# Kernel tuning notes

Measured on AMD Instinct MI355X. Metric: run time of the kernel, lower is better.

Reference implementation:

```python
import jax, jax.numpy as jnp
import numpy as np

D_MODEL = 1024
D_CODEX = 64
CODEX_SIZE = 8192
BETA = 1.0
EPS_NORM = 1e-12
EPS_LN = 1e-5


def l2norm(x):
    # F.normalize(p=2, dim=-1, eps=1e-12): x / max(||x||, eps)
    n = jnp.sqrt(jnp.sum(x * x, axis=-1, keepdims=True))
    return x / jnp.maximum(n, EPS_NORM)


def setup_inputs() -> dict:
    key = jax.random.key(0)
    ks = jax.random.split(key, 8)
    B, S = 4, 2048
    Z = jax.random.normal(ks[0], (B, S, D_MODEL), dtype=jnp.float32)
    W1 = 0.02 * jax.random.normal(ks[1], (D_MODEL, D_MODEL), dtype=jnp.float32)
    b1 = jnp.zeros((D_MODEL,), dtype=jnp.float32)
    W2 = 0.02 * jax.random.normal(ks[2], (D_MODEL, D_CODEX), dtype=jnp.float32)
    b2 = jnp.zeros((D_CODEX,), dtype=jnp.float32)
    codex = l2norm(jax.random.normal(ks[3], (CODEX_SIZE, D_CODEX), dtype=jnp.float32))
    ln_w = jnp.ones((D_CODEX,), dtype=jnp.float32)
    ln_b = jnp.zeros((D_CODEX,), dtype=jnp.float32)
    Wp = 0.02 * jax.random.normal(ks[4], (D_CODEX, D_MODEL), dtype=jnp.float32)
    bp = jnp.zeros((D_MODEL,), dtype=jnp.float32)
    return {"Z": Z, "W1": W1, "b1": b1, "W2": W2, "b2": b2,
            "codex": codex, "ln_w": ln_w, "ln_b": ln_b, "Wp": Wp, "bp": bp}


def reference(Z, W1, b1, W2, b2, codex, ln_w, ln_b, Wp, bp):
    # pre_proj: Linear -> Tanh -> Linear, then l2-normalize into codex space
    Z_e = jnp.tanh(Z @ W1 + b1) @ W2 + b2            # (B, S, d_codex)
    Z_e = l2norm(Z_e)
    flat = Z_e.reshape(-1, D_CODEX)                  # (N, d_codex)
    # squared-L2 distances: |z|^2 + |c|^2 - 2 z.c
    dists = (jnp.sum(flat * flat, axis=-1, keepdims=True)
             + jnp.sum(codex * codex, axis=-1)[None, :]
             - 2.0 * jnp.einsum('nd,cd->nc', flat, codex))  # (N, K)
    idxs = jnp.argmin(dists, axis=-1).reshape(Z_e.shape[:-1])  # (B, S)
    codex_probs = jax.nn.one_hot(idxs, CODEX_SIZE, dtype=Z_e.dtype)  # (B, S, K)
    Z_q = codex[idxs]                                 # (B, S, d_codex)
    # commitment loss (codex is an EMA buffer, no gradient through it)
    loss = BETA * jnp.mean((jax.lax.stop_gradient(Z_q) - Z_e) ** 2)
    # straight-through estimator
    Z_q = Z_e + jax.lax.stop_gradient(Z_q - Z_e)
    # layernorm over d_codex
    mu = jnp.mean(Z_q, axis=-1, keepdims=True)
    var = jnp.mean((Z_q - mu) ** 2, axis=-1, keepdims=True)
    Z_q = (Z_q - mu) * jax.lax.rsqrt(var + EPS_LN) * ln_w + ln_b
    # post_proj back to d_model
    Z_q = Z_q @ Wp + bp                               # (B, S, d_model)
    return Z_q, loss, codex_probs
```

## Files before the change

kernel.cpp:

```cpp
#include <hip/hip_runtime.h>
#include <math.h>
#include <stdint.h>

#define N_TOK   8192
#define DMODEL  1024
#define DCODEX  64
#define KCODES  8192

__global__ __launch_bounds__(256) void codenorm_kernel(const float* __restrict__ codex,
                                                       float* __restrict__ cn2) {
    int k = blockIdx.x * 256 + threadIdx.x;
    const float4* p = (const float4*)(codex + (size_t)k * DCODEX);
    float s = 0.f;
#pragma unroll
    for (int i = 0; i < 16; ++i) {
        float4 v = p[i];
        s += v.x * v.x + v.y * v.y + v.z * v.z + v.w * v.w;
    }
    cn2[k] = s;
}

__global__ __launch_bounds__(256) void gemm1_tanh_kernel(const float* __restrict__ Z,
                                                         const float* __restrict__ W1,
                                                         const float* __restrict__ b1,
                                                         float* __restrict__ H) {
    __shared__ float As[32][132];
    __shared__ float Bs[32][132];
    const int tid = threadIdx.x;
    const int row0 = blockIdx.x * 128;
    const int col0 = blockIdx.y * 128;
    const int ty = tid >> 4, tx = tid & 15;

    float acc[8][8];
#pragma unroll
    for (int i = 0; i < 8; ++i)
#pragma unroll
        for (int j = 0; j < 8; ++j) acc[i][j] = 0.f;

    for (int k0 = 0; k0 < DMODEL; k0 += 32) {
        __syncthreads();
#pragma unroll
        for (int t = 0; t < 4; ++t) {
            int q = tid + t * 256;
            int r = q >> 3, kc = (q & 7) * 4;
            float4 v = *(const float4*)(Z + (size_t)(row0 + r) * DMODEL + k0 + kc);
            As[kc + 0][r] = v.x; As[kc + 1][r] = v.y;
            As[kc + 2][r] = v.z; As[kc + 3][r] = v.w;
        }
#pragma unroll
        for (int t = 0; t < 4; ++t) {
            int q = tid + t * 256;
            int kk = q >> 5, c4 = (q & 31) * 4;
            *(float4*)&Bs[kk][c4] =
                *(const float4*)(W1 + (size_t)(k0 + kk) * DMODEL + col0 + c4);
        }
        __syncthreads();
#pragma unroll
        for (int k = 0; k < 32; ++k) {
            float a[8], b[8];
            *(float4*)&a[0] = *(const float4*)&As[k][ty * 4];
            *(float4*)&a[4] = *(const float4*)&As[k][64 + ty * 4];
            *(float4*)&b[0] = *(const float4*)&Bs[k][tx * 4];
            *(float4*)&b[4] = *(const float4*)&Bs[k][64 + tx * 4];
#pragma unroll
            for (int i = 0; i < 8; ++i)
#pragma unroll
                for (int j = 0; j < 8; ++j)
                    acc[i][j] = fmaf(a[i], b[j], acc[i][j]);
        }
    }

    float bv[8];
    *(float4*)&bv[0] = *(const float4*)(b1 + col0 + tx * 4);
    *(float4*)&bv[4] = *(const float4*)(b1 + col0 + 64 + tx * 4);
#pragma unroll
    for (int half = 0; half < 2; ++half)
#pragma unroll
        for (int i = 0; i < 4; ++i) {
            int r = row0 + half * 64 + ty * 4 + i;
            float o[8];
#pragma unroll
            for (int j = 0; j < 8; ++j) o[j] = tanhf(acc[half * 4 + i][j] + bv[j]);
            *(float4*)(H + (size_t)r * DMODEL + col0 + tx * 4)      = *(float4*)&o[0];
            *(float4*)(H + (size_t)r * DMODEL + col0 + 64 + tx * 4) = *(float4*)&o[4];
        }
}

__global__ __launch_bounds__(256) void gemm2_norm_kernel(const float* __restrict__ H,
                                                         const float* __restrict__ W2,
                                                         const float* __restrict__ b2,
                                                         float* __restrict__ Ze) {
    __shared__ float As[64][36];
    __shared__ float Bs[64][68];
    const int tid = threadIdx.x;
    const int row0 = blockIdx.x * 32;
    const int ty = tid >> 4, tx = tid & 15;

    float acc[2][4];
#pragma unroll
    for (int i = 0; i < 2; ++i)
#pragma unroll
        for (int j = 0; j < 4; ++j) acc[i][j] = 0.f;

    for (int k0 = 0; k0 < DMODEL; k0 += 64) {
        __syncthreads();
#pragma unroll
        for (int t = 0; t < 2; ++t) {
            int q = tid + t * 256;
            int r = q >> 4, k4 = (q & 15) * 4;
            float4 v = *(const float4*)(H + (size_t)(row0 + r) * DMODEL + k0 + k4);
            As[k4 + 0][r] = v.x; As[k4 + 1][r] = v.y;
            As[k4 + 2][r] = v.z; As[k4 + 3][r] = v.w;
        }
#pragma unroll
        for (int t = 0; t < 4; ++t) {
            int q = tid + t * 256;
            int kk = q >> 4, c4 = (q & 15) * 4;
            *(float4*)&Bs[kk][c4] = *(const float4*)(W2 + (size_t)(k0 + kk) * DCODEX + c4);
        }
        __syncthreads();
#pragma unroll
        for (int k = 0; k < 64; ++k) {
            float2 a = *(const float2*)&As[k][ty * 2];
            float4 b = *(const float4*)&Bs[k][tx * 4];
            float bw[4] = {b.x, b.y, b.z, b.w};
#pragma unroll
            for (int j = 0; j < 4; ++j) {
                acc[0][j] = fmaf(a.x, bw[j], acc[0][j]);
                acc[1][j] = fmaf(a.y, bw[j], acc[1][j]);
            }
        }
    }
    float4 b2v4 = *(const float4*)(b2 + tx * 4);
    float b2v[4] = {b2v4.x, b2v4.y, b2v4.z, b2v4.w};
#pragma unroll
    for (int i = 0; i < 2; ++i) {
        float e[4];
#pragma unroll
        for (int j = 0; j < 4; ++j) e[j] = acc[i][j] + b2v[j];
        float ss = e[0] * e[0] + e[1] * e[1] + e[2] * e[2] + e[3] * e[3];
        ss += __shfl_xor(ss, 8, 64);
        ss += __shfl_xor(ss, 4, 64);
        ss += __shfl_xor(ss, 2, 64);
        ss += __shfl_xor(ss, 1, 64);
        float nrm = fmaxf(sqrtf(ss), 1e-12f);
        float o[4];
#pragma unroll
        for (int j = 0; j < 4; ++j) o[j] = e[j] / nrm;
        *(float4*)(Ze + (size_t)(row0 + ty * 2 + i) * DCODEX + tx * 4) = *(float4*)&o[0];
    }
}

__device__ __forceinline__ unsigned fenc(float f) {
    unsigned u = __float_as_uint(f);
    return (u & 0x80000000u) ? ~u : (u | 0x80000000u);
}

__global__ __launch_bounds__(256) void dist_argmin_kernel(const float* __restrict__ Ze,
                                                          const float* __restrict__ codex,
                                                          const float* __restrict__ cn2,
                                                          unsigned long long* __restrict__ gbest) {
    __shared__ float Zs[64][132];
    __shared__ float Cs[32][132];
    __shared__ unsigned long long red[128];
    const int tid = threadIdx.x;
    const int row0 = blockIdx.x * 128;
    const int strip0 = blockIdx.y * 1024;
    const int ty = tid >> 4, tx = tid & 15;

    if (tid < 128) red[tid] = 0xFFFFFFFFFFFFFFFFull;
#pragma unroll
    for (int t = 0; t < 8; ++t) {
        int q = tid + t * 256;
        int r = q >> 4, d4 = (q & 15) * 4;
        float4 v = *(const float4*)(Ze + (size_t)(row0 + r) * DCODEX + d4);
        Zs[d4 + 0][r] = v.x; Zs[d4 + 1][r] = v.y;
        Zs[d4 + 2][r] = v.z; Zs[d4 + 3][r] = v.w;
    }

    float bv[8];
    int bi[8];
#pragma unroll
    for (int i = 0; i < 8; ++i) { bv[i] = INFINITY; bi[i] = 0; }

    for (int c0 = 0; c0 < 1024; c0 += 128) {
        const int cbase = strip0 + c0;
        float cn[8];
        *(float4*)&cn[0] = *(const float4*)(cn2 + cbase + tx * 4);
        *(float4*)&cn[4] = *(const float4*)(cn2 + cbase + 64 + tx * 4);
        float s[8][8];
#pragma unroll
        for (int i = 0; i < 8; ++i)
#pragma unroll
            for (int j = 0; j < 8; ++j) s[i][j] = 0.f;

        for (int h = 0; h < 2; ++h) {
            __syncthreads();
#pragma unroll
            for (int t = 0; t < 4; ++t) {
                int q = tid + t * 256;
                int c = q >> 3, d4 = (q & 7) * 4;
                float4 v = *(const float4*)(codex + (size_t)(cbase + c) * DCODEX + h * 32 + d4);
                Cs[d4 + 0][c] = v.x; Cs[d4 + 1][c] = v.y;
                Cs[d4 + 2][c] = v.z; Cs[d4 + 3][c] = v.w;
            }
            __syncthreads();
#pragma unroll
            for (int d = 0; d < 32; ++d) {
                float a[8], b[8];
                *(float4*)&a[0] = *(const float4*)&Zs[h * 32 + d][ty * 4];
                *(float4*)&a[4] = *(const float4*)&Zs[h * 32 + d][64 + ty * 4];
                *(float4*)&b[0] = *(const float4*)&Cs[d][tx * 4];
                *(float4*)&b[4] = *(const float4*)&Cs[d][64 + tx * 4];
#pragma unroll
                for (int i = 0; i < 8; ++i)
#pragma unroll
                    for (int j = 0; j < 8; ++j)
                        s[i][j] = fmaf(a[i], b[j], s[i][j]);
            }
        }
#pragma unroll
        for (int i = 0; i < 8; ++i)
#pragma unroll
            for (int j = 0; j < 8; ++j) {
                float dist = fmaf(-2.0f, s[i][j], cn[j]);
                int col = cbase + ((j < 4) ? (tx * 4 + j) : (64 + tx * 4 + j - 4));
                if (dist < bv[i]) { bv[i] = dist; bi[i] = col; }
            }
    }
#pragma unroll
    for (int i = 0; i < 8; ++i) {
        int li = (i < 4) ? (ty * 4 + i) : (64 + ty * 4 + i - 4);
        unsigned long long key =
            ((unsigned long long)fenc(bv[i]) << 32) | (unsigned)bi[i];
        atomicMin(&red[li], key);
    }
    __syncthreads();
    if (tid < 128) atomicMin(&gbest[row0 + tid], red[tid]);
}

__global__ __launch_bounds__(256) void scatter_onehot_kernel(const unsigned long long* __restrict__ gbest,
                                                             int* __restrict__ idxbuf,
                                                             float* __restrict__ probs) {
    int n = blockIdx.x * 256 + threadIdx.x;
    unsigned id = (unsigned)(gbest[n] & 0xFFFFFFFFull);
    idxbuf[n] = (int)id;
    probs[(size_t)n * KCODES + id] = 1.0f;
}

__global__ __launch_bounds__(256) void ln_loss_kernel(const int* __restrict__ idxbuf,
                                                      const float* __restrict__ codex,
                                                      const float* __restrict__ Ze,
                                                      const float* __restrict__ ln_w,
                                                      const float* __restrict__ ln_b,
                                                      float* __restrict__ Aln,
                                                      float* __restrict__ loss) {
    const int tid = threadIdx.x;
    const int w = tid >> 6, l = tid & 63;
    const int row = blockIdx.x * 4 + w;
    int id = idxbuf[row];
    float zq = codex[(size_t)id * DCODEX + l];
    float ze = Ze[(size_t)row * DCODEX + l];
    float dlt = zq - ze;
    float val = ze + dlt;
    float s = val;
#pragma unroll
    for (int m = 32; m >= 1; m >>= 1) s += __shfl_xor(s, m, 64);
    float mu = s * 0.015625f;
    float c = val - mu;
    float v2 = c * c;
#pragma unroll
    for (int m = 32; m >= 1; m >>= 1) v2 += __shfl_xor(v2, m, 64);
    float var = v2 * 0.015625f;
    float y = c * (1.0f / sqrtf(var + 1e-5f)) * ln_w[l] + ln_b[l];
    Aln[(size_t)row * DCODEX + l] = y;
    float d2 = dlt * dlt;
#pragma unroll
    for (int m = 32; m >= 1; m >>= 1) d2 += __shfl_xor(d2, m, 64);
    if (l == 0) atomicAdd(loss, d2 * (1.0f / 524288.0f));
}

__global__ __launch_bounds__(256) void gemm3_kernel(const float* __restrict__ Aln,
                                                    const float* __restrict__ Wp,
                                                    const float* __restrict__ bp,
                                                    float* __restrict__ Zq) {
    __shared__ float As[64][132];
    __shared__ float Bs[64][68];
    const int tid = threadIdx.x;
    const int row0 = blockIdx.x * 128;
    const int col0 = blockIdx.y * 64;
    const int ty = tid >> 4, tx = tid & 15;

#pragma unroll
    for (int t = 0; t < 8; ++t) {
        int q = tid + t * 256;
        int r = q >> 4, d4 = (q & 15) * 4;
        float4 v = *(const float4*)(Aln + (size_t)(row0 + r) * DCODEX + d4);
        As[d4 + 0][r] = v.x; As[d4 + 1][r] = v.y;
        As[d4 + 2][r] = v.z; As[d4 + 3][r] = v.w;
    }
#pragma unroll
    for (int t = 0; t < 4; ++t) {
        int q = tid + t * 256;
        int kk = q >> 4, c4 = (q & 15) * 4;
        *(float4*)&Bs[kk][c4] = *(const float4*)(Wp + (size_t)kk * DMODEL + col0 + c4);
    }
    __syncthreads();

    float acc[8][4];
#pragma unroll
    for (int i = 0; i < 8; ++i)
#pragma unroll
        for (int j = 0; j < 4; ++j) acc[i][j] = 0.f;
#pragma unroll
    for (int k = 0; k < 64; ++k) {
        float a[8];
        *(float4*)&a[0] = *(const float4*)&As[k][ty * 4];
        *(float4*)&a[4] = *(const float4*)&As[k][64 + ty * 4];
        float4 b = *(const float4*)&Bs[k][tx * 4];
        float bw[4] = {b.x, b.y, b.z, b.w};
#pragma unroll
        for (int i = 0; i < 8; ++i)
#pragma unroll
            for (int j = 0; j < 4; ++j)
                acc[i][j] = fmaf(a[i], bw[j], acc[i][j]);
    }
    float4 bp4 = *(const float4*)(bp + col0 + tx * 4);
    float bb[4] = {bp4.x, bp4.y, bp4.z, bp4.w};
#pragma unroll
    for (int half = 0; half < 2; ++half)
#pragma unroll
        for (int i = 0; i < 4; ++i) {
            int r = row0 + half * 64 + ty * 4 + i;
            float o[4];
#pragma unroll
            for (int j = 0; j < 4; ++j) o[j] = acc[half * 4 + i][j] + bb[j];
            *(float4*)(Zq + (size_t)r * DMODEL + col0 + tx * 4) = *(float4*)&o[0];
        }
}

extern "C" void kernel_launch(void* const* d_in, const int* in_sizes, int n_in,
                              void* d_out, int out_size, void* d_ws, size_t ws_size,
                              hipStream_t stream) {
    const float* Z     = (const float*)d_in[0];
    const float* W1    = (const float*)d_in[1];
    const float* b1    = (const float*)d_in[2];
    const float* W2    = (const float*)d_in[3];
    const float* b2    = (const float*)d_in[4];
    const float* codex = (const float*)d_in[5];
    const float* ln_w  = (const float*)d_in[6];
    const float* ln_b  = (const float*)d_in[7];
    const float* Wp    = (const float*)d_in[8];
    const float* bp    = (const float*)d_in[9];

    float* out      = (float*)d_out;
    float* Zq_out   = out;
    float* loss_out = out + (size_t)N_TOK * DMODEL;
    float* probs    = loss_out + 1;

    char* ws = (char*)d_ws;
    float* H   = (float*)ws;
    float* Aln = H;
    float* Ze  = H + (size_t)N_TOK * DMODEL;
    float* cn2 = Ze + (size_t)N_TOK * DCODEX;
    unsigned long long* gbest = (unsigned long long*)(cn2 + KCODES);
    int* idxbuf = (int*)(gbest + N_TOK);

    hipMemsetAsync(loss_out, 0, (size_t)(1 + (size_t)N_TOK * KCODES) * sizeof(float), stream);
    hipMemsetAsync(gbest, 0xFF, (size_t)N_TOK * sizeof(unsigned long long), stream);

    codenorm_kernel<<<KCODES / 256, 256, 0, stream>>>(codex, cn2);
    gemm1_tanh_kernel<<<dim3(N_TOK / 128, DMODEL / 128), 256, 0, stream>>>(Z, W1, b1, H);
    gemm2_norm_kernel<<<N_TOK / 32, 256, 0, stream>>>(H, W2, b2, Ze);
    dist_argmin_kernel<<<dim3(N_TOK / 128, KCODES / 1024), 256, 0, stream>>>(Ze, codex, cn2, gbest);
    scatter_onehot_kernel<<<N_TOK / 256, 256, 0, stream>>>(gbest, idxbuf, probs);
    ln_loss_kernel<<<N_TOK / 4, 256, 0, stream>>>(idxbuf, codex, Ze, ln_w, ln_b, Aln, loss_out);
    gemm3_kernel<<<dim3(N_TOK / 128, DMODEL / 64), 256, 0, stream>>>(Aln, Wp, bp, Zq_out);
}
```

Measured before the change: 815.3 us.

## Use split-bf16 MFMA for first GEMM and fuse one-hot zeroing with scatter

Replaces the scalar FP32 first GEMM with a bf16x3 split-precision MFMA kernel. W1 is pre-split into three transposed bf16 tiles by a new kernel, Z is split on the fly, and six MFMA products approximate FP32 accuracy. Separately, the large memset of the one-hot probabilities plus scatter becomes a single kernel that writes each float4 once with the one-hot value in place. The gain is matrix-core throughput for the dominant GEMM and one fewer full pass over the 256MB probs buffer. The cost is extra split arithmetic and a slightly different numerical result that could flip argmin ties.

```diff
diff --git a/kernel.cpp b/kernel.cpp
--- a/kernel.cpp
+++ b/kernel.cpp
@@ -6,6 +6,20 @@
 #define DMODEL  1024
 #define DCODEX  64
 #define KCODES  8192
+
+typedef short short8 __attribute__((ext_vector_type(8)));
+typedef float f32x16 __attribute__((ext_vector_type(16)));
+
+union Frag { short8 s; uint2 u[2]; };
+
+__device__ __forceinline__ unsigned short f2bf(float f) {
+    unsigned u = __float_as_uint(f);
+    unsigned r = u + 0x7FFFu + ((u >> 16) & 1u);
+    return (unsigned short)(r >> 16);
+}
+__device__ __forceinline__ float bf2f(unsigned short h) {
+    return __uint_as_float(((unsigned)h) << 16);
+}
 
 __global__ __launch_bounds__(256) void codenorm_kernel(const float* __restrict__ codex,
                                                        float* __restrict__ cn2) {
@@ -20,22 +34,65 @@
     cn2[k] = s;
 }
 
-__global__ __launch_bounds__(256) void gemm1_tanh_kernel(const float* __restrict__ Z,
-                                                         const float* __restrict__ W1,
+__global__ __launch_bounds__(256) void split_w1_kernel(const float* __restrict__ W1,
+                                                       unsigned short* __restrict__ t0,
+                                                       unsigned short* __restrict__ t1,
+                                                       unsigned short* __restrict__ t2) {
+    __shared__ float tile[32][33];
+    const int tid = threadIdx.x;
+    const int k0 = blockIdx.x * 32;
+    const int n0 = blockIdx.y * 32;
+    {
+        int i = tid >> 3, j4 = (tid & 7) * 4;
+        float4 v = *(const float4*)(W1 + (size_t)(k0 + i) * DMODEL + n0 + j4);
+        tile[i][j4 + 0] = v.x; tile[i][j4 + 1] = v.y;
+        tile[i][j4 + 2] = v.z; tile[i][j4 + 3] = v.w;
+    }
+    __syncthreads();
+    int n = tid >> 3, kq = (tid & 7) * 4;
+    ushort4 h0, h1, h2;
+#pragma unroll
+    for (int c = 0; c < 4; ++c) {
+        float f = tile[kq + c][n];
+        unsigned short a0 = f2bf(f);
+        float r1 = f - bf2f(a0);
+        unsigned short a1 = f2bf(r1);
+        float r2 = r1 - bf2f(a1);
+        unsigned short a2 = f2bf(r2);
+        ((unsigned short*)&h0)[c] = a0;
+        ((unsigned short*)&h1)[c] = a1;
+        ((unsigned short*)&h2)[c] = a2;
+    }
+    size_t off = (size_t)(n0 + n) * DMODEL + k0 + kq;
+    *(ushort4*)(t0 + off) = h0;
+    *(ushort4*)(t1 + off) = h1;
+    *(ushort4*)(t2 + off) = h2;
+}
+
+__global__ __launch_bounds__(256) void gemm1_mfma_kernel(const float* __restrict__ Z,
+                                                         const unsigned short* __restrict__ W1t0,
+                                                         const unsigned short* __restrict__ W1t1,
+                                                         const unsigned short* __restrict__ W1t2,
                                                          const float* __restrict__ b1,
                                                          float* __restrict__ H) {
-    __shared__ float As[32][132];
-    __shared__ float Bs[32][132];
+    __shared__ unsigned short Ash[3][128][36];
+    __shared__ unsigned short Bsh[3][128][36];
     const int tid = threadIdx.x;
     const int row0 = blockIdx.x * 128;
     const int col0 = blockIdx.y * 128;
-    const int ty = tid >> 4, tx = tid & 15;
-
-    float acc[8][8];
-#pragma unroll
-    for (int i = 0; i < 8; ++i)
-#pragma unroll
-        for (int j = 0; j < 8; ++j) acc[i][j] = 0.f;
+    const int wave = tid >> 6;
+    const int lane = tid & 63;
+    const int lrow = lane & 31;
+    const int lhalf = lane >> 5;
+    const int wm = wave >> 1, wn = wave & 1;
+
+    f32x16 acc[2][2];
+#pragma unroll
+    for (int i = 0; i < 2; ++i)
+#pragma unroll
+        for (int j = 0; j < 2; ++j)
+#pragma unroll
+            for (int r = 0; r < 16; ++r) acc[i][j][r] = 0.f;
 
     for (int k0 = 0; k0 < DMODEL; k0 += 32) {
         __syncthreads();
@@ -44,45 +101,87 @@
             int q = tid + t * 256;
             int r = q >> 3, kc = (q & 7) * 4;
             float4 v = *(const float4*)(Z + (size_t)(row0 + r) * DMODEL + k0 + kc);
-            As[kc + 0][r] = v.x; As[kc + 1][r] = v.y;
-            As[kc + 2][r] = v.z; As[kc + 3][r] = v.w;
-        }
-#pragma unroll
-        for (int t = 0; t < 4; ++t) {
-            int q = tid + t * 256;
-            int kk = q >> 5, c4 = (q & 31) * 4;
-            *(float4*)&Bs[kk][c4] =
-                *(const float4*)(W1 + (size_t)(k0 + kk) * DMODEL + col0 + c4);
+            float f[4] = {v.x, v.y, v.z, v.w};
+            unsigned h0[4], h1[4], h2[4];
+#pragma unroll
+            for (int c = 0; c < 4; ++c) {
+                unsigned short a0 = f2bf(f[c]);
+                float r1 = f[c] - bf2f(a0);
+                unsigned short a1 = f2bf(r1);
+                float r2 = r1 - bf2f(a1);
+                unsigned short a2 = f2bf(r2);
+                h0[c] = a0; h1[c] = a1; h2[c] = a2;
+            }
+            uint2 p0 = make_uint2(h0[0] | (h0[1] << 16), h0[2] | (h0[3] << 16));
+            uint2 p1 = make_uint2(h1[0] | (h1[1] << 16), h1[2] | (h1[3] << 16));
+            uint2 p2 = make_uint2(h2[0] | (h2[1] << 16), h2[2] | (h2[3] << 16));
+            *(uint2*)&Ash[0][r][kc] = p0;
+            *(uint2*)&Ash[1][r][kc] = p1;
+            *(uint2*)&Ash[2][r][kc] = p2;
+        }
+#pragma unroll
+        for (int t = 0; t < 6; ++t) {
+            int e = tid + t * 256;
+            int l = e >> 9;
+            int rem = e & 511;
+            int n = rem >> 2, kq = (rem & 3) * 8;
+            const unsigned short* src = (l == 0) ? W1t0 : (l == 1) ? W1t1 : W1t2;
+            uint4 v = *(const uint4*)(src + (size_t)(col0 + n) * DMODEL + k0 + kq);
+            *(uint2*)&Bsh[l][n][kq]     = make_uint2(v.x, v.y);
+            *(uint2*)&Bsh[l][n][kq + 4] = make_uint2(v.z, v.w);
         }
         __syncthreads();
 #pragma unroll
-        for (int k = 0; k < 32; ++k) {
-            float a[8], b[8];
-            *(float4*)&a[0] = *(const float4*)&As[k][ty * 4];
-            *(float4*)&a[4] = *(const float4*)&As[k][64 + ty * 4];
-            *(float4*)&b[0] = *(const float4*)&Bs[k][tx * 4];
-            *(float4*)&b[4] = *(const float4*)&Bs[k][64 + tx * 4];
-#pragma unroll
-            for (int i = 0; i < 8; ++i)
-#pragma unroll
-                for (int j = 0; j < 8; ++j)
-                    acc[i][j] = fmaf(a[i], b[j], acc[i][j]);
-        }
-    }
-
-    float bv[8];
-    *(float4*)&bv[0] = *(const float4*)(b1 + col0 + tx * 4);
-    *(float4*)&bv[4] = *(const float4*)(b1 + col0 + 64 + tx * 4);
-#pragma unroll
-    for (int half = 0; half < 2; ++half)
-#pragma unroll
-        for (int i = 0; i < 4; ++i) {
-            int r = row0 + half * 64 + ty * 4 + i;
-            float o[8];
-#pragma unroll
-            for (int j = 0; j < 8; ++j) o[j] = tanhf(acc[half * 4 + i][j] + bv[j]);
-            *(float4*)(H + (size_t)r * DMODEL + col0 + tx * 4)      = *(float4*)&o[0];
-            *(float4*)(H + (size_t)r * DMODEL + col0 + 64 + tx * 4) = *(float4*)&o[4];
+        for (int mk = 0; mk < 2; ++mk) {
+            const int kb = mk * 16 + lhalf * 8;
+            Frag ah[2], am[2], al[2], bh[2], bm[2], bl[2];
+#pragma unroll
+            for (int ti = 0; ti < 2; ++ti) {
+                int rA = wm * 64 + ti * 32 + lrow;
+                ah[ti].u[0] = *(const uint2*)&Ash[0][rA][kb];
+                ah[ti].u[1] = *(const uint2*)&Ash[0][rA][kb + 4];
+                am[ti].u[0] = *(const uint2*)&Ash[1][rA][kb];
+                am[ti].u[1] = *(const uint2*)&Ash[1][rA][kb + 4];
+                al[ti].u[0] = *(const uint2*)&Ash[2][rA][kb];
+                al[ti].u[1] = *(const uint2*)&Ash[2][rA][kb + 4];
+            }
+#pragma unroll
+            for (int tj = 0; tj < 2; ++tj) {
+                int rB = wn * 64 + tj * 32 + lrow;
+                bh[tj].u[0] = *(const uint2*)&Bsh[0][rB][kb];
+                bh[tj].u[1] = *(const uint2*)&Bsh[0][rB][kb + 4];
+                bm[tj].u[0] = *(const uint2*)&Bsh[1][rB][kb];
+                bm[tj].u[1] = *(const uint2*)&Bsh[1][rB][kb + 4];
+                bl[tj].u[0] = *(const uint2*)&Bsh[2][rB][kb];
+                bl[tj].u[1] = *(const uint2*)&Bsh[2][rB][kb + 4];
+            }
+#pragma unroll
+            for (int ti = 0; ti < 2; ++ti)
+#pragma unroll
+                for (int tj = 0; tj < 2; ++tj) {
+                    acc[ti][tj] = __builtin_amdgcn_mfma_f32_32x32x16_bf16(ah[ti].s, bh[tj].s, acc[ti][tj], 0, 0, 0);
+                    acc[ti][tj] = __builtin_amdgcn_mfma_f32_32x32x16_bf16(ah[ti].s, bm[tj].s, acc[ti][tj], 0, 0, 0);
+                    acc[ti][tj] = __builtin_amdgcn_mfma_f32_32x32x16_bf16(am[ti].s, bh[tj].s, acc[ti][tj], 0, 0, 0);
+                    acc[ti][tj] = __builtin_amdgcn_mfma_f32_32x32x16_bf16(am[ti].s, bm[tj].s, acc[ti][tj], 0, 0, 0);
+                    acc[ti][tj] = __builtin_amdgcn_mfma_f32_32x32x16_bf16(ah[ti].s, bl[tj].s, acc[ti][tj], 0, 0, 0);
+                    acc[ti][tj] = __builtin_amdgcn_mfma_f32_32x32x16_bf16(al[ti].s, bh[tj].s, acc[ti][tj], 0, 0, 0);
+                }
+        }
+    }
+
+    float b1v[2];
+#pragma unroll
+    for (int tj = 0; tj < 2; ++tj) b1v[tj] = b1[col0 + wn * 64 + tj * 32 + lrow];
+#pragma unroll
+    for (int ti = 0; ti < 2; ++ti)
+#pragma unroll
+        for (int tj = 0; tj < 2; ++tj) {
+            int col = col0 + wn * 64 + tj * 32 + lrow;
+#pragma unroll
+            for (int r = 0; r < 16; ++r) {
+                int row = row0 + wm * 64 + ti * 32 + (r & 3) + 8 * (r >> 2) + 4 * lhalf;
+                H[(size_t)row * DMODEL + col] = tanhf(acc[ti][tj][r] + b1v[tj]);
+            }
         }
 }
 
@@ -239,16 +338,18 @@
     if (tid < 128) atomicMin(&gbest[row0 + tid], red[tid]);
 }
 
-__global__ __launch_bounds__(256) void scatter_onehot_kernel(const unsigned long long* __restrict__ gbest,
-                                                             int* __restrict__ idxbuf,
-                                                             float* __restrict__ probs) {
-    int n = blockIdx.x * 256 + threadIdx.x;
-    unsigned id = (unsigned)(gbest[n] & 0xFFFFFFFFull);
-    idxbuf[n] = (int)id;
-    probs[(size_t)n * KCODES + id] = 1.0f;
-}
-
-__global__ __launch_bounds__(256) void ln_loss_kernel(const int* __restrict__ idxbuf,
+__global__ __launch_bounds__(256) void zero_scatter_kernel(const unsigned long long* __restrict__ gbest,
+                                                           float* __restrict__ probs) {
+    size_t g = (size_t)blockIdx.x * 256 + threadIdx.x;
+    int row = (int)(g >> 11);
+    int c4i = (int)(g & 2047);
+    unsigned id = (unsigned)(gbest[row] & 0xFFFFFFFFull);
+    float4 v = {0.f, 0.f, 0.f, 0.f};
+    if ((id >> 2) == (unsigned)c4i) ((float*)&v)[id & 3] = 1.0f;
+    *(float4*)(probs + ((size_t)row << 13) + ((size_t)c4i << 2)) = v;
+}
+
+__global__ __launch_bounds__(256) void ln_loss_kernel(const unsigned long long* __restrict__ gbest,
                                                       const float* __restrict__ codex,
                                                       const float* __restrict__ Ze,
                                                       const float* __restrict__ ln_w,
@@ -258,7 +359,7 @@
     const int tid = threadIdx.x;
     const int w = tid >> 6, l = tid & 63;
     const int row = blockIdx.x * 4 + w;
-    int id = idxbuf[row];
+    int id = (int)(unsigned)(gbest[row] & 0xFFFFFFFFull);
     float zq = codex[(size_t)id * DCODEX + l];
     float ze = Ze[(size_t)row * DCODEX + l];
     float dlt = zq - ze;
@@ -364,16 +465,19 @@
     float* Ze  = H + (size_t)N_TOK * DMODEL;
     float* cn2 = Ze + (size_t)N_TOK * DCODEX;
     unsigned long long* gbest = (unsigned long long*)(cn2 + KCODES);
-    int* idxbuf = (int*)(gbest + N_TOK);
-
-    hipMemsetAsync(loss_out, 0, (size_t)(1 + (size_t)N_TOK * KCODES) * sizeof(float), stream);
+    unsigned short* W1t0 = (unsigned short*)(gbest + N_TOK);
+    unsigned short* W1t1 = W1t0 + (size_t)DMODEL * DMODEL;
+    unsigned short* W1t2 = W1t1 + (size_t)DMODEL * DMODEL;
+
+    hipMemsetAsync(loss_out, 0, sizeof(float), stream);
     hipMemsetAsync(gbest, 0xFF, (size_t)N_TOK * sizeof(unsigned long long), stream);
 
     codenorm_kernel<<<KCODES / 256, 256, 0, stream>>>(codex, cn2);
-    gemm1_tanh_kernel<<<dim3(N_TOK / 128, DMODEL / 128), 256, 0, stream>>>(Z, W1, b1, H);
+    split_w1_kernel<<<dim3(DMODEL / 32, DMODEL / 32), 256, 0, stream>>>(W1, W1t0, W1t1, W1t2);
+    gemm1_mfma_kernel<<<dim3(N_TOK / 128, DMODEL / 128), 256, 0, stream>>>(Z, W1t0, W1t1, W1t2, b1, H);
     gemm2_norm_kernel<<<N_TOK / 32, 256, 0, stream>>>(H, W2, b2, Ze);
     dist_argmin_kernel<<<dim3(N_TOK / 128, KCODES / 1024), 256, 0, stream>>>(Ze, codex, cn2, gbest);
-    scatter_onehot_kernel<<<N_TOK / 256, 256, 0, stream>>>(gbest, idxbuf, probs);
-    ln_loss_kernel<<<N_TOK / 4, 256, 0, stream>>>(idxbuf, codex, Ze, ln_w, ln_b, Aln, loss_out);
+    zero_scatter_kernel<<<(int)(((size_t)N_TOK * KCODES / 4) / 256), 256, 0, stream>>>(gbest, probs);
+    ln_loss_kernel<<<N_TOK / 4, 256, 0, stream>>>(gbest, codex, Ze, ln_w, ln_b, Aln, loss_out);
     gemm3_kernel<<<dim3(N_TOK / 128, DMODEL / 64), 256, 0, stream>>>(Aln, Wp, bp, Zq_out);
 }
```

Measured after the change: 731.5 us. 1.11x faster.
